# Performance work log

Measured on AMD Instinct MI355X. Metric: run time of the kernel, lower is better.

## Reference

```python
import jax, jax.numpy as jnp
import numpy as np

B, S, I, C, P = 64, 14, 32, 10, 4   # batch, spatial, in-caps/pos, classes, pose size
ROUTINGS = 3
EPS = 1e-9


def setup_inputs() -> dict:
    key = jax.random.key(0)
    k1, k2, k3, k4, k5 = jax.random.split(key, 5)
    return {
        "inputs_pose": jax.random.normal(k1, (B, S, S, I, P, P), jnp.float32),
        "inputs_activation": jax.random.uniform(k2, (B, S, S, I), jnp.float32),
        "w": jax.random.normal(k3, (1, I, C, P, P), jnp.float32),
        "beta_v": jax.random.normal(k4, (1, C), jnp.float32) * 0.1,
        "beta_a": jax.random.normal(k5, (1, C), jnp.float32) * 0.1,
    }


def _em_routing(votes, i_act, beta_v, beta_a, routings):
    # votes: [B, N, C, 16], i_act: [B, N]
    Bn, N, Cc, D = votes.shape
    rr = jnp.full((Bn, N, Cc, 1), 1.0 / Cc, votes.dtype)  # uniform init assignments
    bv = beta_v.reshape(1, 1, Cc, 1)
    ba = beta_a.reshape(1, 1, Cc, 1)
    it_min, it_max = 1.0, min(float(routings), 3.0)  # inverse-temperature schedule
    o_mean = o_act = None
    for it in range(routings):
        inv_temp = it_min + (it_max - it_min) * it / max(1.0, routings - 1.0)
        # --- M step ---
        rr_p = rr * i_act[:, :, None, None]                        # [B,N,C,1]
        rr_sum = jnp.sum(rr_p, axis=1, keepdims=True)              # [B,1,C,1]
        o_mean = jnp.sum(rr_p * votes, axis=1, keepdims=True) / rr_sum   # [B,1,C,16]
        o_var = jnp.sum(rr_p * jnp.square(votes - o_mean), axis=1, keepdims=True) / rr_sum
        o_stdv = jnp.sqrt(o_var)                                   # [B,1,C,16]
        cost = jnp.sum((bv + jnp.log(o_stdv + EPS)) * rr_sum, axis=-1, keepdims=True)  # [B,1,C,1]
        o_act = jax.nn.sigmoid(inv_temp * (ba - cost))             # [B,1,C,1]
        # --- E step (skipped on last iteration) ---
        if it < routings - 1:
            logp = (-jnp.sum(jnp.square(votes - o_mean) / (2.0 * jnp.square(o_stdv) + EPS),
                             axis=-1, keepdims=True)
                    - jnp.sum(jnp.log(o_stdv + EPS), axis=-1, keepdims=True))  # [B,N,C,1]
            zz = jnp.log(o_act + EPS) + logp
            rr = jax.nn.softmax(zz, axis=2)
    return o_mean[:, 0], o_act[:, 0, :, 0]  # [B,C,16], [B,C]


def reference(inputs_pose, inputs_activation, w, beta_v, beta_a):
    # mat_transform: votes[b,h,w,i,c] = pose[b,h,w,i] @ W[i,c]   (4x4 matmuls)
    votes = jnp.einsum('bhwipq,icqr->bhwicpr', inputs_pose, w[0])
    votes = votes.reshape(B, S, S, I, C, P * P)
    # coordinate addition: scaled (row+0.5)/S onto pose element 0, col onto element 1
    coord = (jnp.arange(S, dtype=votes.dtype) + 0.5) / S
    votes = votes.at[..., 0].add(coord[None, :, None, None, None])
    votes = votes.at[..., 1].add(coord[None, None, :, None, None])
    votes = votes.reshape(B, S * S * I, C, P * P)
    acts = inputs_activation.reshape(B, S * S * I)
    o_mean, o_act = _em_routing(votes, acts, beta_v, beta_a, ROUTINGS)
    pose = o_mean.reshape(B, C, P, P)
    return pose, o_act
```

## Files before the change

kernel.cpp:

```cpp
#include <hip/hip_runtime.h>
#include <math.h>

#define Bsz 64
#define Ssz 14
#define Isz 32
#define Csz 10
#define Dsz 16
#define Nsz (Ssz*Ssz*Isz)
#define EPSF 1e-9f

#define CH  640
#define NCH 10

__device__ __forceinline__ void compute_vote(const float* __restrict__ p,
                                             const float* __restrict__ Wi,
                                             float chh, float cww, float* v)
{
#pragma unroll
    for (int pr = 0; pr < 4; ++pr)
#pragma unroll
        for (int r = 0; r < 4; ++r)
            v[pr*4+r] = p[pr*4+0]*Wi[0*4+r] + p[pr*4+1]*Wi[1*4+r]
                      + p[pr*4+2]*Wi[2*4+r] + p[pr*4+3]*Wi[3*4+r];
    v[0] += chh;
    v[1] += cww;
}

__global__ __launch_bounds__(640) void m0_kernel(
    const float* __restrict__ pose,
    const float* __restrict__ act,
    const float* __restrict__ w,
    float* __restrict__ partials)
{
    const int b = blockIdx.x, chunk = blockIdx.y;
    const int tid = threadIdx.x, c = tid >> 6, lane = tid & 63;

    __shared__ float Wm[Csz][Isz*17];

    for (int t = tid; t < Csz*Isz*Dsz; t += 640) {
        int cc = t >> 9, rem = t & 511, i = rem >> 4, q = rem & 15;
        Wm[cc][i*17 + q] = w[(i*Csz + cc)*Dsz + q];
    }
    __syncthreads();

    float s0 = 0.f, s1[Dsz], s2[Dsz];
#pragma unroll
    for (int d = 0; d < Dsz; ++d) { s1[d] = 0.f; s2[d] = 0.f; }

    const float* poseb = pose + (size_t)b * Nsz * Dsz;
    const float* actb  = act  + (size_t)b * Nsz;
    const int base = chunk * CH;

    for (int nl = lane; nl < CH; nl += 64) {
        const int n = base + nl;
        if (n < Nsz) {
            const float4* pp = reinterpret_cast<const float4*>(poseb + (size_t)n * Dsz);
            float4 a0 = pp[0], a1 = pp[1], a2 = pp[2], a3 = pp[3];
            float p[16] = {a0.x,a0.y,a0.z,a0.w, a1.x,a1.y,a1.z,a1.w,
                           a2.x,a2.y,a2.z,a2.w, a3.x,a3.y,a3.z,a3.w};
            int i = n & 31, hw = n >> 5;
            int wc = hw % Ssz, hr = hw / Ssz;
            float wgt = actb[n] * (1.0f/Csz);
            float v[16];
            compute_vote(p, &Wm[c][i*17], (hr+0.5f)*(1.0f/Ssz), (wc+0.5f)*(1.0f/Ssz), v);
            s0 += wgt;
#pragma unroll
            for (int d = 0; d < Dsz; ++d) {
                float wv = wgt * v[d];
                s1[d] += wv;
                s2[d] += wv * v[d];
            }
        }
    }

#pragma unroll
    for (int m = 32; m >= 1; m >>= 1) {
        s0 += __shfl_xor(s0, m);
#pragma unroll
        for (int d = 0; d < Dsz; ++d) {
            s1[d] += __shfl_xor(s1[d], m);
            s2[d] += __shfl_xor(s2[d], m);
        }
    }
    if (lane == 0) {
        float* pt = partials + ((size_t)(b*Csz + c)*NCH + chunk)*33;
        pt[0] = s0;
#pragma unroll
        for (int d = 0; d < Dsz; ++d) { pt[1+d] = s1[d]; pt[17+d] = s2[d]; }
    }
}

__global__ __launch_bounds__(640) void em_kernel(
    const float* __restrict__ pose,
    const float* __restrict__ act,
    const float* __restrict__ w,
    const float* __restrict__ beta_v,
    const float* __restrict__ beta_a,
    const float* __restrict__ part_in,
    float* __restrict__ part_out,
    float inv_temp_prev)
{
    const int b = blockIdx.x, chunk = blockIdx.y;
    const int tid = threadIdx.x, wv = tid >> 6, lane = tid & 63;

    __shared__ float Wm[Csz][Isz*17];
    __shared__ float rr[Csz][CH];
    __shared__ float prm[Csz][33];
    __shared__ float Sv[Csz][33];
    __shared__ float lg[Csz][16];

    for (int t = tid; t < Csz*Isz*Dsz; t += 640) {
        int cc = t >> 9, rem = t & 511, i = rem >> 4, q = rem & 15;
        Wm[cc][i*17 + q] = w[(i*Csz + cc)*Dsz + q];
    }
    if (tid < Csz*33) {
        int c = tid / 33, j = tid - c*33;
        const float* pp = part_in + ((size_t)(b*Csz + c)*NCH)*33 + j;
        float s = 0.f;
        for (int ch2 = 0; ch2 < NCH; ++ch2) s += pp[ch2*33];
        Sv[c][j] = s;
    }
    __syncthreads();
    if (tid < Csz*Dsz) {
        int c = tid >> 4, d = tid & 15;
        float S0 = Sv[c][0];
        float mn  = Sv[c][1+d] / S0;
        float var = fmaxf(Sv[c][17+d] / S0 - mn*mn, 0.f);
        float stdv = sqrtf(var);
        prm[c][d]    = mn;
        prm[c][16+d] = 1.f / (2.f*var + EPSF);
        lg[c][d]     = __logf(stdv + EPSF);
    }
    __syncthreads();
    if (tid < Csz) {
        int c = tid;
        float sumlog = 0.f;
#pragma unroll
        for (int d = 0; d < Dsz; ++d) sumlog += lg[c][d];
        float cost = Sv[c][0] * (16.f * beta_v[c] + sumlog);
        float oact = 1.f / (1.f + __expf(-inv_temp_prev * (beta_a[c] - cost)));
        prm[c][32] = __logf(oact + EPSF) - sumlog;
    }
    __syncthreads();

    const int base = chunk * CH;
    const float* poseb = pose + (size_t)b * Nsz * Dsz;
    {
        const int n = base + tid;
        if (n < Nsz) {
            const float4* pp = reinterpret_cast<const float4*>(poseb + (size_t)n * Dsz);
            float4 a0 = pp[0], a1 = pp[1], a2 = pp[2], a3 = pp[3];
            float p[16] = {a0.x,a0.y,a0.z,a0.w, a1.x,a1.y,a1.z,a1.w,
                           a2.x,a2.y,a2.z,a2.w, a3.x,a3.y,a3.z,a3.w};
            int i = n & 31, hw = n >> 5;
            int wc = hw % Ssz, hr = hw / Ssz;
            float chh = (hr+0.5f)*(1.0f/Ssz), cww = (wc+0.5f)*(1.0f/Ssz);
            float a = act[(size_t)b*Nsz + n];

            float zz[Csz];
#pragma unroll
            for (int c = 0; c < Csz; ++c) {
                float v[16];
                compute_vote(p, &Wm[c][i*17], chh, cww, v);
                float quad = 0.f;
#pragma unroll
                for (int d = 0; d < Dsz; ++d) {
                    float dv = v[d] - prm[c][d];
                    quad += dv * dv * prm[c][16+d];
                }
                zz[c] = prm[c][32] - quad;
            }
            float zmax = zz[0];
#pragma unroll
            for (int c = 1; c < Csz; ++c) zmax = fmaxf(zmax, zz[c]);
            float zsum = 0.f;
#pragma unroll
            for (int c = 0; c < Csz; ++c) { zz[c] = __expf(zz[c] - zmax); zsum += zz[c]; }
            float sc = __fdividef(a, zsum);
#pragma unroll
            for (int c = 0; c < Csz; ++c) rr[c][tid] = zz[c] * sc;
        }
    }
    __syncthreads();

    const int c = wv;
    float s0 = 0.f, s1[Dsz], s2[Dsz];
#pragma unroll
    for (int d = 0; d < Dsz; ++d) { s1[d] = 0.f; s2[d] = 0.f; }

    for (int nl = lane; nl < CH; nl += 64) {
        const int n = base + nl;
        if (n < Nsz) {
            const float4* pp = reinterpret_cast<const float4*>(poseb + (size_t)n * Dsz);
            float4 a0 = pp[0], a1 = pp[1], a2 = pp[2], a3 = pp[3];
            float p[16] = {a0.x,a0.y,a0.z,a0.w, a1.x,a1.y,a1.z,a1.w,
                           a2.x,a2.y,a2.z,a2.w, a3.x,a3.y,a3.z,a3.w};
            int i = n & 31, hw = n >> 5;
            int wc = hw % Ssz, hr = hw / Ssz;
            float wgt = rr[c][nl];
            float v[16];
            compute_vote(p, &Wm[c][i*17], (hr+0.5f)*(1.0f/Ssz), (wc+0.5f)*(1.0f/Ssz), v);
            s0 += wgt;
#pragma unroll
            for (int d = 0; d < Dsz; ++d) {
                float wvv = wgt * v[d];
                s1[d] += wvv;
                s2[d] += wvv * v[d];
            }
        }
    }

#pragma unroll
    for (int m = 32; m >= 1; m >>= 1) {
        s0 += __shfl_xor(s0, m);
#pragma unroll
        for (int d = 0; d < Dsz; ++d) {
            s1[d] += __shfl_xor(s1[d], m);
            s2[d] += __shfl_xor(s2[d], m);
        }
    }
    if (lane == 0) {
        float* pt = part_out + ((size_t)(b*Csz + c)*NCH + chunk)*33;
        pt[0] = s0;
#pragma unroll
        for (int d = 0; d < Dsz; ++d) { pt[1+d] = s1[d]; pt[17+d] = s2[d]; }
    }
}

__global__ __launch_bounds__(64) void fin_kernel(
    const float* __restrict__ partials,
    const float* __restrict__ beta_v,
    const float* __restrict__ beta_a,
    float* __restrict__ out,
    float inv_temp)
{
    const int bc = blockIdx.x * 64 + threadIdx.x;
    if (bc >= Bsz*Csz) return;
    const int c = bc % Csz;

    float S[33];
#pragma unroll
    for (int j = 0; j < 33; ++j) S[j] = 0.f;
    const float* pb = partials + (size_t)bc * NCH * 33;
    for (int ch2 = 0; ch2 < NCH; ++ch2)
#pragma unroll
        for (int j = 0; j < 33; ++j) S[j] += pb[ch2*33 + j];

    float S0 = S[0], rS0 = 1.f / S0;
    float sumlog = 0.f;
    float* om = out + (size_t)bc * Dsz;
#pragma unroll
    for (int d = 0; d < Dsz; ++d) {
        float mn  = S[1+d] * rS0;
        float var = fmaxf(S[17+d] * rS0 - mn*mn, 0.f);
        sumlog += __logf(sqrtf(var) + EPSF);
        om[d] = mn;
    }
    float cost = S0 * (16.f * beta_v[c] + sumlog);
    float oact = 1.f / (1.f + __expf(-inv_temp * (beta_a[c] - cost)));
    out[Bsz*Csz*Dsz + bc] = oact;
}

extern "C" void kernel_launch(void* const* d_in, const int* in_sizes, int n_in,
                              void* d_out, int out_size, void* d_ws, size_t ws_size,
                              hipStream_t stream)
{
    const float* pose = (const float*)d_in[0];
    const float* act  = (const float*)d_in[1];
    const float* w    = (const float*)d_in[2];
    const float* bv   = (const float*)d_in[3];
    const float* ba   = (const float*)d_in[4];
    float* out = (float*)d_out;

    float* partA = (float*)d_ws;
    float* partB = partA + (size_t)Bsz*Csz*NCH*33;

    dim3 grid(Bsz, NCH);

    m0_kernel<<<grid, CH, 0, stream>>>(pose, act, w, partA);
    em_kernel<<<grid, CH, 0, stream>>>(pose, act, w, bv, ba, partA, partB, 1.0f);
    em_kernel<<<grid, CH, 0, stream>>>(pose, act, w, bv, ba, partB, partA, 2.0f);
    fin_kernel<<<(Bsz*Csz + 63)/64, 64, 0, stream>>>(partA, bv, ba, out, 3.0f);
}
```

Measured before the change: 224.2 us.

## Compute first M-step from per-capsule pose moments and hoist parameter finalization

The first M step uses uniform routing weights, so it now accumulates activation-weighted pose moments per input-capsule type (first and second order, plus coordinate cross terms) without forming votes. A small kernel then maps those moments through W to per-class means and variances. Parameter finalization moves out of the EM kernel into separate small kernels that write precomputed mean, inverse-variance and log terms, so each EM block no longer reduces the partials itself. The accumulation loop keeps W for the lane's capsule in registers and reduces with DPP row operations. The cost is more kernel launches, heavy register and LDS-atomic use in the moment kernel, and the precision risk of computing variance from raw moments.

```diff
diff --git a/kernel.cpp b/kernel.cpp
--- a/kernel.cpp
+++ b/kernel.cpp
@@ -9,166 +9,210 @@
 #define Nsz (Ssz*Ssz*Isz)
 #define EPSF 1e-9f
 
-#define CH  640
-#define NCH 10
-
-__device__ __forceinline__ void compute_vote(const float* __restrict__ p,
-                                             const float* __restrict__ Wi,
-                                             float chh, float cww, float* v)
-{
-#pragma unroll
-    for (int pr = 0; pr < 4; ++pr)
-#pragma unroll
-        for (int r = 0; r < 4; ++r)
-            v[pr*4+r] = p[pr*4+0]*Wi[0*4+r] + p[pr*4+1]*Wi[1*4+r]
-                      + p[pr*4+2]*Wi[2*4+r] + p[pr*4+3]*Wi[3*4+r];
-    v[0] += chh;
-    v[1] += cww;
-}
-
-__global__ __launch_bounds__(640) void m0_kernel(
+#define CH   640
+#define NCH  10
+#define MCH  3136
+#define PST  36
+#define MST  72
+
+template<int CTRL, int RMASK>
+__device__ __forceinline__ float dpp_add(float x) {
+    int y = __builtin_amdgcn_update_dpp(0, __float_as_int(x), CTRL, RMASK, 0xf, true);
+    return x + __int_as_float(y);
+}
+__device__ __forceinline__ float wave_sum64(float x) {
+    x = dpp_add<0x111, 0xf>(x);
+    x = dpp_add<0x112, 0xf>(x);
+    x = dpp_add<0x114, 0xf>(x);
+    x = dpp_add<0x118, 0xf>(x);
+    x = dpp_add<0x142, 0xa>(x);
+    x = dpp_add<0x143, 0xc>(x);
+    return x;
+}
+
+__global__ __launch_bounds__(640) void mom_kernel(
     const float* __restrict__ pose,
     const float* __restrict__ act,
-    const float* __restrict__ w,
-    float* __restrict__ partials)
-{
-    const int b = blockIdx.x, chunk = blockIdx.y;
-    const int tid = threadIdx.x, c = tid >> 6, lane = tid & 63;
-
-    __shared__ float Wm[Csz][Isz*17];
-
-    for (int t = tid; t < Csz*Isz*Dsz; t += 640) {
-        int cc = t >> 9, rem = t & 511, i = rem >> 4, q = rem & 15;
-        Wm[cc][i*17 + q] = w[(i*Csz + cc)*Dsz + q];
-    }
-    __syncthreads();
-
-    float s0 = 0.f, s1[Dsz], s2[Dsz];
-#pragma unroll
-    for (int d = 0; d < Dsz; ++d) { s1[d] = 0.f; s2[d] = 0.f; }
-
-    const float* poseb = pose + (size_t)b * Nsz * Dsz;
-    const float* actb  = act  + (size_t)b * Nsz;
-    const int base = chunk * CH;
-
-    for (int nl = lane; nl < CH; nl += 64) {
-        const int n = base + nl;
-        if (n < Nsz) {
-            const float4* pp = reinterpret_cast<const float4*>(poseb + (size_t)n * Dsz);
+    float* __restrict__ partM)
+{
+    const int b = blockIdx.x, mch = blockIdx.y;
+    const int tid = threadIdx.x, lane = tid & 63;
+
+    __shared__ float Macc[32][73];
+
+    float s[69];
+#pragma unroll
+    for (int j = 0; j < 69; ++j) s[j] = 0.f;
+
+    const float* poseb = pose + (size_t)b*Nsz*Dsz;
+    const float* actb  = act  + (size_t)b*Nsz;
+    const int base = mch*MCH;
+
+    for (int k = 0; k < MCH; k += 640) {
+        const int nl = k + tid;
+        if (nl < MCH) {
+            const int n = base + nl;
+            const float4* pp = reinterpret_cast<const float4*>(poseb + (size_t)n*Dsz);
             float4 a0 = pp[0], a1 = pp[1], a2 = pp[2], a3 = pp[3];
             float p[16] = {a0.x,a0.y,a0.z,a0.w, a1.x,a1.y,a1.z,a1.w,
                            a2.x,a2.y,a2.z,a2.w, a3.x,a3.y,a3.z,a3.w};
-            int i = n & 31, hw = n >> 5;
-            int wc = hw % Ssz, hr = hw / Ssz;
-            float wgt = actb[n] * (1.0f/Csz);
-            float v[16];
-            compute_vote(p, &Wm[c][i*17], (hr+0.5f)*(1.0f/Ssz), (wc+0.5f)*(1.0f/Ssz), v);
-            s0 += wgt;
-#pragma unroll
-            for (int d = 0; d < Dsz; ++d) {
-                float wv = wgt * v[d];
-                s1[d] += wv;
-                s2[d] += wv * v[d];
+            const int hw = n >> 5;
+            const int wc = hw % Ssz, hr = hw / Ssz;
+            const float chh = (hr+0.5f)*(1.0f/Ssz), cww = (wc+0.5f)*(1.0f/Ssz);
+            const float wgt = actb[n]*(1.0f/Csz);
+            s[0] += wgt;
+            float wp[16];
+#pragma unroll
+            for (int j = 0; j < 16; ++j) { wp[j] = wgt*p[j]; s[1+j] += wp[j]; }
+            int t = 17;
+#pragma unroll
+            for (int pr = 0; pr < 4; ++pr)
+#pragma unroll
+                for (int k1 = 0; k1 < 4; ++k1)
+#pragma unroll
+                    for (int k2 = k1; k2 < 4; ++k2)
+                        s[t++] += wp[pr*4+k1]*p[pr*4+k2];
+            const float wch = wgt*chh, wcw = wgt*cww;
+#pragma unroll
+            for (int j = 0; j < 4; ++j) { s[57+j] += wch*p[j]; s[61+j] += wcw*p[j]; }
+            s[65] += wch; s[66] += wcw; s[67] += wch*chh; s[68] += wcw*cww;
+        }
+    }
+#pragma unroll
+    for (int j = 0; j < 69; ++j) s[j] += __shfl_xor(s[j], 32);
+
+    for (int t = tid; t < 32*73; t += 640) (&Macc[0][0])[t] = 0.f;
+    __syncthreads();
+    if (lane < 32) {
+#pragma unroll
+        for (int j = 0; j < 69; ++j) atomicAdd(&Macc[lane][j], s[j]);
+    }
+    __syncthreads();
+    float* ob = partM + (size_t)(b*2 + mch)*32*MST;
+    for (int t = tid; t < 32*MST; t += 640) {
+        const int i = t / MST, j = t - i*MST;
+        ob[t] = (j < 69) ? Macc[i][j] : 0.f;
+    }
+}
+
+__global__ __launch_bounds__(256) void fin0_kernel(
+    const float* __restrict__ partM,
+    const float* __restrict__ w,
+    const float* __restrict__ beta_v, const float* __restrict__ beta_a,
+    float* __restrict__ prm, float inv_temp)
+{
+    const int b = blockIdx.x, tid = threadIdx.x;
+    __shared__ float Mr[32][73];
+    __shared__ float Ws[Isz*Csz*Dsz];
+    __shared__ float pm[Csz][16], pg[Csz][16], pl[Csz][16];
+    __shared__ float s0sh;
+
+    const float* p0 = partM + (size_t)(b*2 + 0)*32*MST;
+    const float* p1 = partM + (size_t)(b*2 + 1)*32*MST;
+    for (int t = tid; t < 32*MST; t += 256) {
+        const int i = t / MST, j = t - i*MST;
+        Mr[i][j] = p0[t] + p1[t];
+    }
+    for (int t = tid; t < Isz*Csz*Dsz; t += 256) Ws[t] = w[t];
+    __syncthreads();
+
+    if (tid < Csz*Dsz) {
+        const int c = tid >> 4, d = tid & 15, pr = d >> 2, r = d & 3;
+        float S0 = 0.f, S1 = 0.f, S2 = 0.f;
+        for (int i = 0; i < 32; ++i) {
+            const float* Wi = Ws + (i*Csz + c)*Dsz;
+            const float* Mi = Mr[i];
+            S0 += Mi[0];
+            const float w0 = Wi[0*4+r], w1 = Wi[1*4+r], w2 = Wi[2*4+r], w3 = Wi[3*4+r];
+            const float* M1 = Mi + 1 + pr*4;
+            S1 += w0*M1[0] + w1*M1[1] + w2*M1[2] + w3*M1[3];
+            const float* Q = Mi + 17 + pr*10;
+            S2 += w0*w0*Q[0] + w1*w1*Q[4] + w2*w2*Q[7] + w3*w3*Q[9]
+                + 2.f*(w0*w1*Q[1] + w0*w2*Q[2] + w0*w3*Q[3]
+                     + w1*w2*Q[5] + w1*w3*Q[6] + w2*w3*Q[8]);
+            if (d == 0) {
+                S1 += Mi[65];
+                S2 += 2.f*(w0*Mi[57] + w1*Mi[58] + w2*Mi[59] + w3*Mi[60]) + Mi[67];
+            } else if (d == 1) {
+                S1 += Mi[66];
+                S2 += 2.f*(w0*Mi[61] + w1*Mi[62] + w2*Mi[63] + w3*Mi[64]) + Mi[68];
             }
         }
-    }
-
-#pragma unroll
-    for (int m = 32; m >= 1; m >>= 1) {
-        s0 += __shfl_xor(s0, m);
-#pragma unroll
-        for (int d = 0; d < Dsz; ++d) {
-            s1[d] += __shfl_xor(s1[d], m);
-            s2[d] += __shfl_xor(s2[d], m);
-        }
-    }
-    if (lane == 0) {
-        float* pt = partials + ((size_t)(b*Csz + c)*NCH + chunk)*33;
-        pt[0] = s0;
-#pragma unroll
-        for (int d = 0; d < Dsz; ++d) { pt[1+d] = s1[d]; pt[17+d] = s2[d]; }
+        const float mean = S1 / S0;
+        const float var = fmaxf(S2/S0 - mean*mean, 0.f);
+        pm[c][d] = mean;
+        pg[c][d] = 1.f/(2.f*var + EPSF);
+        pl[c][d] = __logf(sqrtf(var) + EPSF);
+        if (tid == 0) s0sh = S0;
+    }
+    __syncthreads();
+    if (tid < Csz) {
+        const int c = tid;
+        float sumlog = 0.f;
+#pragma unroll
+        for (int d = 0; d < 16; ++d) sumlog += pl[c][d];
+        const float cost = s0sh*(16.f*beta_v[c] + sumlog);
+        const float oact = 1.f/(1.f + __expf(-inv_temp*(beta_a[c] - cost)));
+        const float K = __logf(oact + EPSF) - sumlog;
+        float* o = prm + (size_t)(b*Csz + c)*PST;
+#pragma unroll
+        for (int d = 0; d < 16; ++d) { o[d] = pm[c][d]; o[16+d] = pg[c][d]; }
+        o[32] = K;
     }
 }
 
 __global__ __launch_bounds__(640) void em_kernel(
-    const float* __restrict__ pose,
-    const float* __restrict__ act,
-    const float* __restrict__ w,
-    const float* __restrict__ beta_v,
-    const float* __restrict__ beta_a,
-    const float* __restrict__ part_in,
-    float* __restrict__ part_out,
-    float inv_temp_prev)
+    const float* __restrict__ pose, const float* __restrict__ act,
+    const float* __restrict__ w, const float* __restrict__ prm,
+    float* __restrict__ partC)
 {
     const int b = blockIdx.x, chunk = blockIdx.y;
     const int tid = threadIdx.x, wv = tid >> 6, lane = tid & 63;
 
     __shared__ float Wm[Csz][Isz*17];
     __shared__ float rr[Csz][CH];
-    __shared__ float prm[Csz][33];
-    __shared__ float Sv[Csz][33];
-    __shared__ float lg[Csz][16];
 
     for (int t = tid; t < Csz*Isz*Dsz; t += 640) {
-        int cc = t >> 9, rem = t & 511, i = rem >> 4, q = rem & 15;
+        const int cc = t >> 9, rem = t & 511, i = rem >> 4, q = rem & 15;
         Wm[cc][i*17 + q] = w[(i*Csz + cc)*Dsz + q];
     }
-    if (tid < Csz*33) {
-        int c = tid / 33, j = tid - c*33;
-        const float* pp = part_in + ((size_t)(b*Csz + c)*NCH)*33 + j;
-        float s = 0.f;
-        for (int ch2 = 0; ch2 < NCH; ++ch2) s += pp[ch2*33];
-        Sv[c][j] = s;
-    }
-    __syncthreads();
-    if (tid < Csz*Dsz) {
-        int c = tid >> 4, d = tid & 15;
-        float S0 = Sv[c][0];
-        float mn  = Sv[c][1+d] / S0;
-        float var = fmaxf(Sv[c][17+d] / S0 - mn*mn, 0.f);
-        float stdv = sqrtf(var);
-        prm[c][d]    = mn;
-        prm[c][16+d] = 1.f / (2.f*var + EPSF);
-        lg[c][d]     = __logf(stdv + EPSF);
-    }
-    __syncthreads();
-    if (tid < Csz) {
-        int c = tid;
-        float sumlog = 0.f;
-#pragma unroll
-        for (int d = 0; d < Dsz; ++d) sumlog += lg[c][d];
-        float cost = Sv[c][0] * (16.f * beta_v[c] + sumlog);
-        float oact = 1.f / (1.f + __expf(-inv_temp_prev * (beta_a[c] - cost)));
-        prm[c][32] = __logf(oact + EPSF) - sumlog;
-    }
-    __syncthreads();
-
-    const int base = chunk * CH;
-    const float* poseb = pose + (size_t)b * Nsz * Dsz;
+    __syncthreads();
+
+    const int base = chunk*CH;
+    const float* poseb = pose + (size_t)b*Nsz*Dsz;
+
     {
         const int n = base + tid;
         if (n < Nsz) {
-            const float4* pp = reinterpret_cast<const float4*>(poseb + (size_t)n * Dsz);
+            const float4* pp = reinterpret_cast<const float4*>(poseb + (size_t)n*Dsz);
             float4 a0 = pp[0], a1 = pp[1], a2 = pp[2], a3 = pp[3];
             float p[16] = {a0.x,a0.y,a0.z,a0.w, a1.x,a1.y,a1.z,a1.w,
                            a2.x,a2.y,a2.z,a2.w, a3.x,a3.y,a3.z,a3.w};
-            int i = n & 31, hw = n >> 5;
-            int wc = hw % Ssz, hr = hw / Ssz;
-            float chh = (hr+0.5f)*(1.0f/Ssz), cww = (wc+0.5f)*(1.0f/Ssz);
-            float a = act[(size_t)b*Nsz + n];
-
+            const int i = tid & 31;
+            const int hw = n >> 5;
+            const int wc = hw % Ssz, hr = hw / Ssz;
+            const float chh = (hr+0.5f)*(1.0f/Ssz), cww = (wc+0.5f)*(1.0f/Ssz);
+            const float a = act[(size_t)b*Nsz + n];
             float zz[Csz];
 #pragma unroll
             for (int c = 0; c < Csz; ++c) {
-                float v[16];
-                compute_vote(p, &Wm[c][i*17], chh, cww, v);
+                const float* __restrict__ Wi = &Wm[c][i*17];
+                const float* __restrict__ pg = prm + (size_t)(b*Csz + c)*PST;
                 float quad = 0.f;
 #pragma unroll
-                for (int d = 0; d < Dsz; ++d) {
-                    float dv = v[d] - prm[c][d];
-                    quad += dv * dv * prm[c][16+d];
+                for (int pr = 0; pr < 4; ++pr) {
+#pragma unroll
+                    for (int r = 0; r < 4; ++r) {
+                        float vv = p[pr*4+0]*Wi[0*4+r] + p[pr*4+1]*Wi[1*4+r]
+                                 + p[pr*4+2]*Wi[2*4+r] + p[pr*4+3]*Wi[3*4+r];
+                        if (pr == 0 && r == 0) vv += chh;
+                        if (pr == 0 && r == 1) vv += cww;
+                        const int d = pr*4 + r;
+                        const float dv = vv - pg[d];
+                        quad += dv*dv*pg[16+d];
+                    }
                 }
-                zz[c] = prm[c][32] - quad;
+                zz[c] = pg[32] - quad;
             }
             float zmax = zz[0];
 #pragma unroll
@@ -176,89 +220,102 @@
             float zsum = 0.f;
 #pragma unroll
             for (int c = 0; c < Csz; ++c) { zz[c] = __expf(zz[c] - zmax); zsum += zz[c]; }
-            float sc = __fdividef(a, zsum);
-#pragma unroll
-            for (int c = 0; c < Csz; ++c) rr[c][tid] = zz[c] * sc;
+            const float sc = __fdividef(a, zsum);
+#pragma unroll
+            for (int c = 0; c < Csz; ++c) rr[c][tid] = zz[c]*sc;
         }
     }
     __syncthreads();
 
     const int c = wv;
-    float s0 = 0.f, s1[Dsz], s2[Dsz];
-#pragma unroll
-    for (int d = 0; d < Dsz; ++d) { s1[d] = 0.f; s2[d] = 0.f; }
-
-    for (int nl = lane; nl < CH; nl += 64) {
+    float W16[16];
+#pragma unroll
+    for (int j = 0; j < 16; ++j) W16[j] = Wm[c][(lane & 31)*17 + j];
+
+    float s0 = 0.f, s1[16], s2[16];
+#pragma unroll
+    for (int d = 0; d < 16; ++d) { s1[d] = 0.f; s2[d] = 0.f; }
+
+    for (int k = 0; k < CH; k += 64) {
+        const int nl = k + lane;
         const int n = base + nl;
         if (n < Nsz) {
-            const float4* pp = reinterpret_cast<const float4*>(poseb + (size_t)n * Dsz);
-            float4 a0 = pp[0], a1 = pp[1], a2 = pp[2], a3 = pp[3];
-            float p[16] = {a0.x,a0.y,a0.z,a0.w, a1.x,a1.y,a1.z,a1.w,
-                           a2.x,a2.y,a2.z,a2.w, a3.x,a3.y,a3.z,a3.w};
-            int i = n & 31, hw = n >> 5;
-            int wc = hw % Ssz, hr = hw / Ssz;
-            float wgt = rr[c][nl];
-            float v[16];
-            compute_vote(p, &Wm[c][i*17], (hr+0.5f)*(1.0f/Ssz), (wc+0.5f)*(1.0f/Ssz), v);
+            const float4* pp = reinterpret_cast<const float4*>(poseb + (size_t)n*Dsz);
+            const int hw = n >> 5;
+            const int wc2 = hw % Ssz, hr2 = hw / Ssz;
+            const float chh = (hr2+0.5f)*(1.0f/Ssz), cww = (wc2+0.5f)*(1.0f/Ssz);
+            const float wgt = rr[c][nl];
             s0 += wgt;
 #pragma unroll
-            for (int d = 0; d < Dsz; ++d) {
-                float wvv = wgt * v[d];
-                s1[d] += wvv;
-                s2[d] += wvv * v[d];
+            for (int pr = 0; pr < 4; ++pr) {
+                const float4 pv = pp[pr];
+#pragma unroll
+                for (int r = 0; r < 4; ++r) {
+                    float vv = pv.x*W16[0*4+r] + pv.y*W16[1*4+r]
+                             + pv.z*W16[2*4+r] + pv.w*W16[3*4+r];
+                    if (pr == 0 && r == 0) vv += chh;
+                    if (pr == 0 && r == 1) vv += cww;
+                    const float wvv = wgt*vv;
+                    s1[pr*4+r] += wvv;
+                    s2[pr*4+r] += wvv*vv;
+                }
             }
         }
     }
-
-#pragma unroll
-    for (int m = 32; m >= 1; m >>= 1) {
-        s0 += __shfl_xor(s0, m);
-#pragma unroll
-        for (int d = 0; d < Dsz; ++d) {
-            s1[d] += __shfl_xor(s1[d], m);
-            s2[d] += __shfl_xor(s2[d], m);
-        }
-    }
-    if (lane == 0) {
-        float* pt = part_out + ((size_t)(b*Csz + c)*NCH + chunk)*33;
+    s0 = wave_sum64(s0);
+#pragma unroll
+    for (int d = 0; d < 16; ++d) { s1[d] = wave_sum64(s1[d]); s2[d] = wave_sum64(s2[d]); }
+    if (lane == 63) {
+        const int bc = b*Csz + c;
+        float* pt = partC + (size_t)chunk*33*(Bsz*Csz) + bc;
         pt[0] = s0;
 #pragma unroll
-        for (int d = 0; d < Dsz; ++d) { pt[1+d] = s1[d]; pt[17+d] = s2[d]; }
-    }
-}
-
-__global__ __launch_bounds__(64) void fin_kernel(
-    const float* __restrict__ partials,
-    const float* __restrict__ beta_v,
-    const float* __restrict__ beta_a,
-    float* __restrict__ out,
-    float inv_temp)
-{
-    const int bc = blockIdx.x * 64 + threadIdx.x;
-    if (bc >= Bsz*Csz) return;
+        for (int d = 0; d < 16; ++d) {
+            pt[(size_t)(1+d)*(Bsz*Csz)]  = s1[d];
+            pt[(size_t)(17+d)*(Bsz*Csz)] = s2[d];
+        }
+    }
+}
+
+__global__ __launch_bounds__(64) void fin12_kernel(
+    const float* __restrict__ partC, const float* __restrict__ beta_v,
+    const float* __restrict__ beta_a, float* __restrict__ prm,
+    float* __restrict__ out, float inv_temp)
+{
+    const int bc = blockIdx.x*64 + threadIdx.x;
     const int c = bc % Csz;
-
     float S[33];
 #pragma unroll
     for (int j = 0; j < 33; ++j) S[j] = 0.f;
-    const float* pb = partials + (size_t)bc * NCH * 33;
-    for (int ch2 = 0; ch2 < NCH; ++ch2)
-#pragma unroll
-        for (int j = 0; j < 33; ++j) S[j] += pb[ch2*33 + j];
-
-    float S0 = S[0], rS0 = 1.f / S0;
+    for (int ch = 0; ch < NCH; ++ch) {
+        const float* pb = partC + (size_t)ch*33*(Bsz*Csz) + bc;
+#pragma unroll
+        for (int j = 0; j < 33; ++j) S[j] += pb[(size_t)j*(Bsz*Csz)];
+    }
+    const float S0 = S[0], rS0 = 1.f/S0;
+    float mean[16], gv[16];
     float sumlog = 0.f;
-    float* om = out + (size_t)bc * Dsz;
-#pragma unroll
-    for (int d = 0; d < Dsz; ++d) {
-        float mn  = S[1+d] * rS0;
-        float var = fmaxf(S[17+d] * rS0 - mn*mn, 0.f);
+#pragma unroll
+    for (int d = 0; d < 16; ++d) {
+        const float mn = S[1+d]*rS0;
+        const float var = fmaxf(S[17+d]*rS0 - mn*mn, 0.f);
+        mean[d] = mn;
+        gv[d] = 1.f/(2.f*var + EPSF);
         sumlog += __logf(sqrtf(var) + EPSF);
-        om[d] = mn;
-    }
-    float cost = S0 * (16.f * beta_v[c] + sumlog);
-    float oact = 1.f / (1.f + __expf(-inv_temp * (beta_a[c] - cost)));
-    out[Bsz*Csz*Dsz + bc] = oact;
+    }
+    const float cost = S0*(16.f*beta_v[c] + sumlog);
+    const float oact = 1.f/(1.f + __expf(-inv_temp*(beta_a[c] - cost)));
+    if (out) {
+#pragma unroll
+        for (int d = 0; d < 16; ++d) out[(size_t)bc*16 + d] = mean[d];
+        out[(size_t)Bsz*Csz*Dsz + bc] = oact;
+    } else {
+        const float K = __logf(oact + EPSF) - sumlog;
+        float* o = prm + (size_t)bc*PST;
+#pragma unroll
+        for (int d = 0; d < 16; ++d) { o[d] = mean[d]; o[16+d] = gv[d]; }
+        o[32] = K;
+    }
 }
 
 extern "C" void kernel_launch(void* const* d_in, const int* in_sizes, int n_in,
@@ -272,13 +329,15 @@
     const float* ba   = (const float*)d_in[4];
     float* out = (float*)d_out;
 
-    float* partA = (float*)d_ws;
-    float* partB = partA + (size_t)Bsz*Csz*NCH*33;
-
-    dim3 grid(Bsz, NCH);
-
-    m0_kernel<<<grid, CH, 0, stream>>>(pose, act, w, partA);
-    em_kernel<<<grid, CH, 0, stream>>>(pose, act, w, bv, ba, partA, partB, 1.0f);
-    em_kernel<<<grid, CH, 0, stream>>>(pose, act, w, bv, ba, partB, partA, 2.0f);
-    fin_kernel<<<(Bsz*Csz + 63)/64, 64, 0, stream>>>(partA, bv, ba, out, 3.0f);
-}
+    float* partM = (float*)d_ws;
+    float* partC = partM;
+    float* prmA  = partM + (size_t)Bsz*2*32*MST;
+    float* prmB  = prmA + (size_t)Bsz*Csz*PST;
+
+    mom_kernel  <<<dim3(Bsz, 2),   640, 0, stream>>>(pose, act, partM);
+    fin0_kernel <<<Bsz,            256, 0, stream>>>(partM, w, bv, ba, prmA, 1.0f);
+    em_kernel   <<<dim3(Bsz, NCH), 640, 0, stream>>>(pose, act, w, prmA, partC);
+    fin12_kernel<<<(Bsz*Csz)/64,    64, 0, stream>>>(partC, bv, ba, prmB, nullptr, 2.0f);
+    em_kernel   <<<dim3(Bsz, NCH), 640, 0, stream>>>(pose, act, w, prmB, partC);
+    fin12_kernel<<<(Bsz*Csz)/64,    64, 0, stream>>>(partC, bv, ba, nullptr, out, 3.0f);
+}
```

After: 254.7 us. +13.6%, slower.
